# Kernel tuning notes

Hardware: AMD Instinct MI355X
Metric: run time of the kernel (lower is better)

## Reference

```python
import jax, jax.numpy as jnp
import numpy as np

N_NODES = 50000
N_EDGES = 800000
D = 64


def _gcn_conv(x, row, col, edge_weight, W, b):
    # degree via scatter-add of edge weights onto source nodes (row)
    deg = jax.ops.segment_sum(edge_weight, row, num_segments=x.shape[0])
    deg_inv_sqrt = jnp.where(deg > 0, jax.lax.rsqrt(deg), 0.0)  # inf -> 0
    norm = deg_inv_sqrt[row] * edge_weight * deg_inv_sqrt[col]  # [E]
    h = x @ W + b                                               # [N, out]
    msg = norm[:, None] * h[row]                                # gather + scale, [E, out]
    # PyG 'add' aggregation onto target nodes (col)
    return jax.ops.segment_sum(msg, col, num_segments=x.shape[0])


def setup_inputs() -> dict:
    key = jax.random.key(0)
    ks = jax.random.split(key, 5)
    x = jax.random.normal(ks[0], (N_NODES, D), dtype=jnp.float32)
    edge_index = jax.random.randint(ks[1], (2, N_EDGES), 0, N_NODES, dtype=jnp.int64)
    edge_weight = jax.random.uniform(ks[2], (N_EDGES,), dtype=jnp.float32)
    s = 1.0 / np.sqrt(D)
    W1 = jax.random.normal(ks[3], (D, D), dtype=jnp.float32) * s
    b1 = jnp.zeros((D,), dtype=jnp.float32)
    W2 = jax.random.normal(ks[4], (D, D), dtype=jnp.float32) * s
    b2 = jnp.zeros((D,), dtype=jnp.float32)
    return {"x": x, "edge_index": edge_index, "edge_weight": edge_weight,
            "W1": W1, "b1": b1, "W2": W2, "b2": b2}


def reference(x, edge_index, edge_weight, W1, b1, W2, b2):
    row, col = edge_index[0], edge_index[1]
    h = _gcn_conv(x, row, col, edge_weight, W1, b1)
    h = jax.nn.relu(h)  # dropout is identity in eval mode
    h = _gcn_conv(h, row, col, edge_weight, W2, b2)
    return h
```

## Files before the change

### kernel.cpp

```cpp
#include <hip/hip_runtime.h>
#include <hip/hip_fp16.h>

#define NNODES 50000
#define NEDGES 800000
#define DIM 64
#define CAP 64

#define NBUCK 196
#define EPB 3200
#define NCH 250
#define MAXB 6144
#define CASTB (NNODES * 16 / 256)
#define GROUPS (NNODES / 8)

#define POISON_I ((int)0xAAAAAAAA)

__global__ __launch_bounds__(256) void pA(const int* __restrict__ ei,
                                          const float* __restrict__ ew,
                                          unsigned int* __restrict__ gbc,
                                          unsigned int* __restrict__ gbr,
                                          unsigned long long* __restrict__ recc,
                                          unsigned long long* __restrict__ recr,
                                          const float* __restrict__ x,
                                          __half* __restrict__ xs) {
    int tid = threadIdx.x, bid = blockIdx.x;
    if (bid >= NCH) {
        int i = (bid - NCH) * 256 + tid;
        float4 v = ((const float4*)x)[i];
        __half2 p0 = __float22half2_rn(make_float2(v.x, v.y));
        __half2 p1 = __float22half2_rn(make_float2(v.z, v.w));
        uint2 u;
        u.x = *(unsigned int*)&p0;
        u.y = *(unsigned int*)&p1;
        ((uint2*)xs)[i] = u;
        return;
    }
    __shared__ unsigned int hc[NBUCK], hr[NBUCK];
    __shared__ unsigned int bc[NBUCK], br[NBUCK];
    if (tid < NBUCK) { hc[tid] = 0u; hr[tid] = 0u; }
    __syncthreads();
    int base = bid * EPB;
    for (int i = tid; i < EPB; i += 256) {
        int r = ei[base + i];
        int c = ei[NEDGES + base + i];
        atomicAdd(&hc[c >> 8], 1u);
        atomicAdd(&hr[r >> 8], 1u);
    }
    __syncthreads();
    if (tid < NBUCK) {
        bc[tid] = atomicAdd(&gbc[tid], hc[tid]) - (unsigned int)POISON_I;
        br[tid] = atomicAdd(&gbr[tid], hr[tid]) - (unsigned int)POISON_I;
    }
    __syncthreads();
    for (int i = tid; i < EPB; i += 256) {
        int r = ei[base + i];
        int c = ei[NEDGES + base + i];
        float w = ew[base + i];
        unsigned int hw = (unsigned int)__half_as_ushort(__float2half(w));
        unsigned int pc = atomicAdd(&bc[c >> 8], 1u);
        recc[(size_t)(c >> 8) * MAXB + pc] =
            (unsigned long long)(unsigned int)r |
            ((unsigned long long)(c & 255) << 16) |
            ((unsigned long long)hw << 32);
        unsigned int pr = atomicAdd(&br[r >> 8], 1u);
        recr[(size_t)(r >> 8) * MAXB + pr] =
            (unsigned long long)(r & 255) |
            ((unsigned long long)__float_as_uint(w) << 32);
    }
}

__global__ __launch_bounds__(256) void p4_build(const unsigned long long* __restrict__ recc,
                                                const unsigned long long* __restrict__ recr,
                                                const unsigned int* __restrict__ gbc,
                                                const unsigned int* __restrict__ gbr,
                                                unsigned int* __restrict__ edata,
                                                int* __restrict__ cnt,
                                                float* __restrict__ deg) {
    int bid = blockIdx.x, tid = threadIdx.x;
    if (bid < NBUCK) {
        __shared__ unsigned int c256[256];
        c256[tid] = 0u;
        __syncthreads();
        int n = (int)(gbc[bid] - (unsigned int)POISON_I);
        const unsigned long long* rb = recc + (size_t)bid * MAXB;
        for (int i = tid; i < n; i += 256) {
            unsigned long long rec = rb[i];
            unsigned int r = (unsigned int)rec & 0xFFFFu;
            unsigned int cl = ((unsigned int)rec >> 16) & 0xFFu;
            unsigned int hw = (unsigned int)(rec >> 32) & 0xFFFFu;
            unsigned int pos = atomicAdd(&c256[cl], 1u);
            if (pos < CAP) edata[(unsigned)((bid << 8) + cl) * CAP + pos] = r | (hw << 16);
        }
        __syncthreads();
        int node = (bid << 8) + tid;
        if (node < NNODES) cnt[node] = (int)c256[tid];
    } else {
        int b = bid - NBUCK;
        __shared__ float d256[256];
        d256[tid] = 0.f;
        __syncthreads();
        int n = (int)(gbr[b] - (unsigned int)POISON_I);
        const unsigned long long* rb = recr + (size_t)b * MAXB;
        for (int i = tid; i < n; i += 256) {
            unsigned long long rec = rb[i];
            atomicAdd(&d256[(unsigned int)rec & 0xFFu],
                      __uint_as_float((unsigned int)(rec >> 32)));
        }
        __syncthreads();
        int node = (b << 8) + tid;
        if (node < NNODES) deg[node] = d256[tid];
    }
}

__device__ __forceinline__ void store_out(__half* O, int i, float v) {
    O[i] = __float2half(v);
}
__device__ __forceinline__ void store_out(float* O, int i, float v) { O[i] = v; }

__device__ __forceinline__ float rsq0(float d) {
    return (d > 0.f) ? rsqrtf(d) : 0.f;
}

template <bool IS_L1, typename OutT>
__global__ __launch_bounds__(256) void layer_kernel(const int* __restrict__ cnt,
                                                    const unsigned int* __restrict__ edata,
                                                    const __half* __restrict__ HS,
                                                    const float* __restrict__ deg,
                                                    float* __restrict__ qbuf,
                                                    const float* __restrict__ W,
                                                    const float* __restrict__ b,
                                                    OutT* __restrict__ O) {
    __shared__ float Wsh[64 * 64];
    __shared__ float Ls[8][64];

    const int tid = threadIdx.x;
    {
        const float4* Wv = (const float4*)W;
        float4* Wd = (float4*)Wsh;
#pragma unroll
        for (int i = 0; i < 4; i++) Wd[tid + 256 * i] = Wv[tid + 256 * i];
    }

    const int wave = tid >> 6;
    const int lane = tid & 63;
    const int h = lane >> 5;
    const int hl = lane & 31;
    const int sub = hl >> 3;
    const int sl = hl & 7;
    const int hbit = lane & 32;
    const uint4* __restrict__ H16 = (const uint4*)HS;
    const float blane = b[lane];

    const int na = blockIdx.x * 8 + wave * 2;
    const int node = na + h;

    int m = cnt[node];
    if (m > CAP) m = CAP;
    unsigned int dw = 0, dw2 = 0;
    if (hl < m) dw = edata[node * CAP + hl];
    if (32 + hl < m) dw2 = edata[node * CAP + 32 + hl];

    float acc[8];
#pragma unroll
    for (int k = 0; k < 8; k++) acc[k] = 0.f;
    float p = 0.f;

    int mm;
    {
        int mo = __shfl_xor(m, 32);
        mm = (mo > m) ? mo : m;
    }

    unsigned int uA0 = 0, uB0 = 0, uA1 = 0, uB1 = 0;
    uint4 hA0, hB0, hA1, hB1;
    float fA0 = 0.f, fB0 = 0.f, fA1 = 0.f, fB1 = 0.f;

    auto issue = [&](unsigned int dwx, int j, unsigned int& uA, unsigned int& uB,
                     uint4& hA, uint4& hB, float& fA, float& fB) {
        uA = (unsigned int)__shfl((int)dwx, hbit | (8 * j + sub));
        uB = (unsigned int)__shfl((int)dwx, hbit | (8 * j + 4 + sub));
        int rA = (int)(uA & 0xFFFFu), rB = (int)(uB & 0xFFFFu);
        hA = H16[rA * 8 + sl];
        hB = H16[rB * 8 + sl];
        if (IS_L1) { fA = deg[rA]; fB = deg[rB]; }
    };
    auto consume = [&](unsigned int uA, unsigned int uB, uint4 hA, uint4 hB,
                       float fA, float fB) {
        float ndA = __half2float(__ushort_as_half((unsigned short)(uA >> 16)));
        float ndB = __half2float(__ushort_as_half((unsigned short)(uB >> 16)));
        if (IS_L1) {
            ndA *= rsq0(fA);
            ndB *= rsq0(fB);
            p += ndA + ndB;
        }
        const __half2* cA = (const __half2*)&hA;
        const __half2* cB = (const __half2*)&hB;
#pragma unroll
        for (int k = 0; k < 4; k++) {
            float2 f0 = __half22float2(cA[k]);
            float2 f1 = __half22float2(cB[k]);
            acc[2 * k + 0] = fmaf(ndA, f0.x, acc[2 * k + 0]);
            acc[2 * k + 1] = fmaf(ndA, f0.y, acc[2 * k + 1]);
            acc[2 * k + 0] = fmaf(ndB, f1.x, acc[2 * k + 0]);
            acc[2 * k + 1] = fmaf(ndB, f1.y, acc[2 * k + 1]);
        }
    };

    {
        int nu = (((mm < 32) ? mm : 32) + 7) >> 3;
        if (nu > 0) {
            issue(dw, 0, uA0, uB0, hA0, hB0, fA0, fB0);
            if (nu > 1) issue(dw, 1, uA1, uB1, hA1, hB1, fA1, fB1);
            consume(uA0, uB0, hA0, hB0, fA0, fB0);
            if (nu > 2) issue(dw, 2, uA0, uB0, hA0, hB0, fA0, fB0);
            if (nu > 1) consume(uA1, uB1, hA1, hB1, fA1, fB1);
            if (nu > 3) issue(dw, 3, uA1, uB1, hA1, hB1, fA1, fB1);
            if (nu > 2) consume(uA0, uB0, hA0, hB0, fA0, fB0);
            if (nu > 3) consume(uA1, uB1, hA1, hB1, fA1, fB1);
        }
    }
    if (mm > 32) {
        int nu2 = ((mm - 32) + 7) >> 3;
        issue(dw2, 0, uA0, uB0, hA0, hB0, fA0, fB0);
        if (nu2 > 1) issue(dw2, 1, uA1, uB1, hA1, hB1, fA1, fB1);
        consume(uA0, uB0, hA0, hB0, fA0, fB0);
        if (nu2 > 2) issue(dw2, 2, uA0, uB0, hA0, hB0, fA0, fB0);
        if (nu2 > 1) consume(uA1, uB1, hA1, hB1, fA1, fB1);
        if (nu2 > 3) issue(dw2, 3, uA1, uB1, hA1, hB1, fA1, fB1);
        if (nu2 > 2) consume(uA0, uB0, hA0, hB0, fA0, fB0);
        if (nu2 > 3) consume(uA1, uB1, hA1, hB1, fA1, fB1);
    }

#pragma unroll
    for (int mask = 8; mask <= 16; mask <<= 1) {
#pragma unroll
        for (int k = 0; k < 8; k++) acc[k] += __shfl_xor(acc[k], mask);
        if (IS_L1) p += __shfl_xor(p, mask);
    }

    if (sub == 0) {
        *(float4*)&Ls[wave * 2 + h][8 * sl + 0] = make_float4(acc[0], acc[1], acc[2], acc[3]);
        *(float4*)&Ls[wave * 2 + h][8 * sl + 4] = make_float4(acc[4], acc[5], acc[6], acc[7]);
    }

    float qa, qb;
    if (IS_L1) {
        qa = __shfl(p, 0);
        qb = __shfl(p, 32);
        if (lane == 0) qbuf[na] = qa;
        if (lane == 32) qbuf[na + 1] = qb;
    } else {
        qa = qbuf[na];
        qb = qbuf[na + 1];
    }
    __syncthreads();

    float oa = qa * blane;
    float ob = qb * blane;
#pragma unroll
    for (int f4 = 0; f4 < 16; f4++) {
        float4 Aa = *(const float4*)&Ls[wave * 2 + 0][4 * f4];
        float4 Ab = *(const float4*)&Ls[wave * 2 + 1][4 * f4];
        float w0 = Wsh[(4 * f4 + 0) * 64 + lane];
        float w1 = Wsh[(4 * f4 + 1) * 64 + lane];
        float w2 = Wsh[(4 * f4 + 2) * 64 + lane];
        float w3 = Wsh[(4 * f4 + 3) * 64 + lane];
        oa = fmaf(Aa.x, w0, oa); ob = fmaf(Ab.x, w0, ob);
        oa = fmaf(Aa.y, w1, oa); ob = fmaf(Ab.y, w1, ob);
        oa = fmaf(Aa.z, w2, oa); ob = fmaf(Ab.z, w2, ob);
        oa = fmaf(Aa.w, w3, oa); ob = fmaf(Ab.w, w3, ob);
    }

    float da = rsq0(deg[na]);
    float db = rsq0(deg[na + 1]);
    float za = da * oa, zb = db * ob;
    if (IS_L1) {
        za = fmaxf(za, 0.f);
        zb = fmaxf(zb, 0.f);
        store_out(O, na * DIM + lane, da * za);
        store_out(O, (na + 1) * DIM + lane, db * zb);
    } else {
        store_out(O, na * DIM + lane, za);
        store_out(O, (na + 1) * DIM + lane, zb);
    }
}

extern "C" void kernel_launch(void* const* d_in, const int* in_sizes, int n_in,
                              void* d_out, int out_size, void* d_ws, size_t ws_size,
                              hipStream_t stream) {
    const float* x  = (const float*)d_in[0];
    const int*   ei = (const int*)d_in[1];
    const float* ew = (const float*)d_in[2];
    const float* W1 = (const float*)d_in[3];
    const float* b1 = (const float*)d_in[4];
    const float* W2 = (const float*)d_in[5];
    const float* b2 = (const float*)d_in[6];
    float* out = (float*)d_out;

    const int N = NNODES;

    char* ws = (char*)d_ws;
    size_t off = 0;
    auto alloc = [&](size_t bytes) { char* p = ws + off; off += (bytes + 255) & ~size_t(255); return p; };
    float*        deg   = (float*)alloc((size_t)N * 4);
    int*          cnt   = (int*)  alloc((size_t)N * 4);
    unsigned int* edata = (unsigned int*)alloc((size_t)N * CAP * 4);
    float*        qbuf  = (float*)alloc((size_t)N * 4);
    __half*       xs    = (__half*)alloc((size_t)N * DIM * 2);
    __half*       h1s   = (__half*)alloc((size_t)N * DIM * 2);
    unsigned int* gbc   = (unsigned int*)alloc((size_t)NBUCK * 4);
    unsigned int* gbr   = (unsigned int*)alloc((size_t)NBUCK * 4);
    unsigned long long* recr = (unsigned long long*)alloc((size_t)NBUCK * MAXB * 8);
    unsigned long long* recc = (unsigned long long*)d_out;

    pA<<<NCH + CASTB, 256, 0, stream>>>(ei, ew, gbc, gbr, recc, recr, x, xs);
    p4_build<<<2 * NBUCK, 256, 0, stream>>>(recc, recr, gbc, gbr, edata, cnt, deg);

    layer_kernel<true, __half><<<GROUPS, 256, 0, stream>>>(cnt, edata, xs, deg, qbuf, W1, b1, h1s);
    layer_kernel<false, float><<<GROUPS, 256, 0, stream>>>(cnt, edata, h1s, deg, qbuf, W2, b2, out);
}
```

Measured before the change: 158.9 us.

## Stage bucketed edge records in shared memory for coalesced scatter and edata writes

The partition kernel now computes a block-local prefix sum over bucket counts, places each record into a bucket-sorted shared-memory staging array, and then writes records to global memory in contiguous runs per bucket. This replaces random per-edge scattered 8-byte stores. The build kernel assembles each bucket's 256×CAP adjacency image in shared memory and copies it out with coalesced uint4 stores, and the edata allocation is padded to a whole number of buckets. The cost is much larger shared-memory use (about 38KB in pA and 64KB in p4_build), which lowers occupancy, plus extra barriers for the scans. The full image copy also writes unused slots.

```diff
diff --git a/kernel.cpp b/kernel.cpp
--- a/kernel.cpp
+++ b/kernel.cpp
@@ -36,7 +36,13 @@
         return;
     }
     __shared__ unsigned int hc[NBUCK], hr[NBUCK];
-    __shared__ unsigned int bc[NBUCK], br[NBUCK];
+    __shared__ unsigned int bcb[NBUCK], brb[NBUCK];
+    __shared__ unsigned int lb[256];
+    __shared__ unsigned int cur[NBUCK];
+    __shared__ unsigned int off[NBUCK];
+    __shared__ unsigned long long stage[EPB];
+    __shared__ unsigned int gidx[EPB];
+
     if (tid < NBUCK) { hc[tid] = 0u; hr[tid] = 0u; }
     __syncthreads();
     int base = bid * EPB;
@@ -48,8 +54,23 @@
     }
     __syncthreads();
     if (tid < NBUCK) {
-        bc[tid] = atomicAdd(&gbc[tid], hc[tid]) - (unsigned int)POISON_I;
-        br[tid] = atomicAdd(&gbr[tid], hr[tid]) - (unsigned int)POISON_I;
+        bcb[tid] = atomicAdd(&gbc[tid], hc[tid]) - (unsigned int)POISON_I;
+        brb[tid] = atomicAdd(&gbr[tid], hr[tid]) - (unsigned int)POISON_I;
+    }
+
+    lb[tid] = (tid < NBUCK) ? hc[tid] : 0u;
+    __syncthreads();
+#pragma unroll
+    for (int d = 1; d < 256; d <<= 1) {
+        unsigned int v = (tid >= d) ? lb[tid - d] : 0u;
+        __syncthreads();
+        lb[tid] += v;
+        __syncthreads();
+    }
+    if (tid < NBUCK) {
+        unsigned int eb = lb[tid] - hc[tid];
+        cur[tid] = eb;
+        off[tid] = (unsigned int)(tid * MAXB) + bcb[tid] - eb;
     }
     __syncthreads();
     for (int i = tid; i < EPB; i += 256) {
@@ -57,16 +78,43 @@
         int c = ei[NEDGES + base + i];
         float w = ew[base + i];
         unsigned int hw = (unsigned int)__half_as_ushort(__float2half(w));
-        unsigned int pc = atomicAdd(&bc[c >> 8], 1u);
-        recc[(size_t)(c >> 8) * MAXB + pc] =
-            (unsigned long long)(unsigned int)r |
-            ((unsigned long long)(c & 255) << 16) |
-            ((unsigned long long)hw << 32);
-        unsigned int pr = atomicAdd(&br[r >> 8], 1u);
-        recr[(size_t)(r >> 8) * MAXB + pr] =
-            (unsigned long long)(r & 255) |
-            ((unsigned long long)__float_as_uint(w) << 32);
-    }
+        int b = c >> 8;
+        unsigned int s = atomicAdd(&cur[b], 1u);
+        stage[s] = (unsigned long long)(unsigned int)r |
+                   ((unsigned long long)(c & 255) << 16) |
+                   ((unsigned long long)hw << 32);
+        gidx[s] = off[b] + s;
+    }
+    __syncthreads();
+    for (int i = tid; i < EPB; i += 256) recc[gidx[i]] = stage[i];
+    __syncthreads();
+
+    lb[tid] = (tid < NBUCK) ? hr[tid] : 0u;
+    __syncthreads();
+#pragma unroll
+    for (int d = 1; d < 256; d <<= 1) {
+        unsigned int v = (tid >= d) ? lb[tid - d] : 0u;
+        __syncthreads();
+        lb[tid] += v;
+        __syncthreads();
+    }
+    if (tid < NBUCK) {
+        unsigned int eb = lb[tid] - hr[tid];
+        cur[tid] = eb;
+        off[tid] = (unsigned int)(tid * MAXB) + brb[tid] - eb;
+    }
+    __syncthreads();
+    for (int i = tid; i < EPB; i += 256) {
+        int r = ei[base + i];
+        float w = ew[base + i];
+        int b = r >> 8;
+        unsigned int s = atomicAdd(&cur[b], 1u);
+        stage[s] = (unsigned long long)(unsigned int)(r & 255) |
+                   ((unsigned long long)__float_as_uint(w) << 32);
+        gidx[s] = off[b] + s;
+    }
+    __syncthreads();
+    for (int i = tid; i < EPB; i += 256) recr[gidx[i]] = stage[i];
 }
 
 __global__ __launch_bounds__(256) void p4_build(const unsigned long long* __restrict__ recc,
@@ -78,6 +126,7 @@
                                                 float* __restrict__ deg) {
     int bid = blockIdx.x, tid = threadIdx.x;
     if (bid < NBUCK) {
+        __shared__ unsigned int img[256 * CAP];
         __shared__ unsigned int c256[256];
         c256[tid] = 0u;
         __syncthreads();
@@ -89,11 +138,15 @@
             unsigned int cl = ((unsigned int)rec >> 16) & 0xFFu;
             unsigned int hw = (unsigned int)(rec >> 32) & 0xFFFFu;
             unsigned int pos = atomicAdd(&c256[cl], 1u);
-            if (pos < CAP) edata[(unsigned)((bid << 8) + cl) * CAP + pos] = r | (hw << 16);
+            if (pos < CAP) img[(cl << 6) + pos] = r | (hw << 16);
         }
         __syncthreads();
         int node = (bid << 8) + tid;
         if (node < NNODES) cnt[node] = (int)c256[tid];
+        const uint4* src = (const uint4*)img;
+        uint4* dst = (uint4*)(edata + ((size_t)bid << 8) * CAP);
+#pragma unroll
+        for (int k = 0; k < 16; k++) dst[k * 256 + tid] = src[k * 256 + tid];
     } else {
         int b = bid - NBUCK;
         __shared__ float d256[256];
@@ -304,7 +357,7 @@
     auto alloc = [&](size_t bytes) { char* p = ws + off; off += (bytes + 255) & ~size_t(255); return p; };
     float*        deg   = (float*)alloc((size_t)N * 4);
     int*          cnt   = (int*)  alloc((size_t)N * 4);
-    unsigned int* edata = (unsigned int*)alloc((size_t)N * CAP * 4);
+    unsigned int* edata = (unsigned int*)alloc((size_t)NBUCK * 256 * CAP * 4);
     float*        qbuf  = (float*)alloc((size_t)N * 4);
     __half*       xs    = (__half*)alloc((size_t)N * DIM * 2);
     __half*       h1s   = (__half*)alloc((size_t)N * DIM * 2);
```

Result: no change. 158.3 us (-0.3%).
